# Kernel tuning notes

Measured on AMD Instinct MI355X. Metric: run time of the kernel, lower is better.

The kernel has to match this reference:

```python
import jax, jax.numpy as jnp
import numpy as np

B, N, DIM = 4, 2048, 512
H, DH = 8, 64  # n_heads, dim_head; inner = H*DH = 512
SCALE = DH ** -0.5


def setup_inputs() -> dict:
    key = jax.random.key(0)
    k1, k2, k3 = jax.random.split(key, 3)
    inner = H * DH
    X = jax.random.normal(k1, (B, N, DIM), dtype=jnp.float32)
    W_qkv = jax.random.normal(k2, (DIM, 3 * inner), dtype=jnp.float32) * (DIM ** -0.5)
    W_out = jax.random.normal(k3, (inner, DIM), dtype=jnp.float32) * (inner ** -0.5)
    b_out = jnp.zeros((DIM,), dtype=jnp.float32)
    return {"X": X, "W_qkv": W_qkv, "W_out": W_out, "b_out": b_out}


def reference(X, W_qkv, W_out, b_out):
    # X: (b, n, dim)
    qkv = X @ W_qkv                      # (b, n, 3*h*d)
    q, k, v = jnp.split(qkv, 3, axis=-1)
    def to_heads(t):
        b, n, _ = t.shape
        return t.reshape(b, n, H, DH).transpose(0, 2, 1, 3)  # (b, h, n, d)
    q, k, v = to_heads(q), to_heads(k), to_heads(v)
    # NOTE: original computes scores[n, m] = k_n . q_m and softmaxes over m (query axis)
    scores = jnp.einsum('bhnd,bhmd->bhnm', k, q) * SCALE     # (b, h, n_k, m_q)
    att = jax.nn.softmax(scores, axis=-1)
    # out token axis is the KEY index n: out[n, d] = sum_e att[n, e] * v[e, d]
    out = jnp.einsum('bhne,bhed->bhnd', att, v)              # (b, h, n, d)
    out = out.transpose(0, 2, 1, 3).reshape(X.shape[0], X.shape[1], H * DH)  # (b, n, h*d)
    return out @ W_out + b_out
```

## Files before the change

kernel.cpp:

```cpp
#include <hip/hip_runtime.h>
#include <hip/hip_bf16.h>

typedef __bf16 bf16_t;
typedef bf16_t bf16x8 __attribute__((ext_vector_type(8)));
typedef bf16_t bf16x4v __attribute__((ext_vector_type(4)));
typedef float f32x4 __attribute__((ext_vector_type(4)));
typedef float f32x16 __attribute__((ext_vector_type(16)));
typedef int i32x4 __attribute__((ext_vector_type(4)));

#define B_SZ 4
#define N_TOK 2048
#define DIM 512
#define H_N 8
#define DH 64
#define INNER 512
#define M_ROWS 8192
#define NQKV 1536
#define K_FOLD 0.18033688011112042f

#define GLD_LDS16(gp, lp)                                          \
  __builtin_amdgcn_global_load_lds(                                \
      (const __attribute__((address_space(1))) void*)(gp),         \
      (__attribute__((address_space(3))) void*)(lp), 16, 0, 0)

__device__ __forceinline__ float fexp2(float x) {
#if __has_builtin(__builtin_amdgcn_exp2f)
  return __builtin_amdgcn_exp2f(x);
#else
  float r;
  asm volatile("v_exp_f32 %0, %1\n\ts_nop 1" : "=v"(r) : "v"(x));
  return r;
#endif
}

__device__ __forceinline__ int cvtpk_bf16(float lo, float hi) {
  int r;
  asm("v_cvt_pk_bf16_f32 %0, %1, %2" : "=v"(r) : "v"(lo), "v"(hi));
  return r;
}

__device__ __forceinline__ void permswap32(int& a, int& b) {
  asm volatile("v_permlane32_swap_b32 %0, %1" : "+v"(a), "+v"(b));
}

#define XJOB 1048576
#define WQJOB 786432
#define WOJOB 262144
__global__ void prep_kernel(const float* __restrict__ X, bf16_t* __restrict__ Xb,
                            const float* __restrict__ Wqkv, bf16_t* __restrict__ WqkvT,
                            const float* __restrict__ Wout, bf16_t* __restrict__ WoutT) {
  int i = blockIdx.x * blockDim.x + threadIdx.x;
  if (i < XJOB) {
    float4 f = reinterpret_cast<const float4*>(X)[i];
    bf16x4v o;
    o.x = (bf16_t)f.x; o.y = (bf16_t)f.y; o.z = (bf16_t)f.z; o.w = (bf16_t)f.w;
    reinterpret_cast<bf16x4v*>(Xb)[i] = o;
  } else if (i < XJOB + WQJOB) {
    int t = i - XJOB;
    int r = t / NQKV, c = t - r * NQKV;
    WqkvT[(size_t)c * DIM + r] = (bf16_t)Wqkv[t];
  } else if (i < XJOB + WQJOB + WOJOB) {
    int t = i - (XJOB + WQJOB);
    int r = t >> 9, c = t & 511;
    WoutT[(size_t)c * INNER + r] = (bf16_t)Wout[t];
  }
}

__global__ __launch_bounds__(256) void gemm_qkv_kernel(
    const bf16_t* __restrict__ A, const bf16_t* __restrict__ Bt, int K,
    bf16_t* __restrict__ qb, bf16_t* __restrict__ kb, bf16_t* __restrict__ vtb) {
  __shared__ bf16_t As[128 * 64];
  __shared__ bf16_t Bs[128 * 64];

  const int tid = threadIdx.x;
  const int lane = tid & 63;
  const int wave = tid >> 6;
  const int g = lane >> 4, c = lane & 15;
  const int wm = (wave >> 1) * 64, wn = (wave & 1) * 64;
  const int m0 = blockIdx.x * 128, n0 = blockIdx.y * 128;

  f32x4 acc[4][4] = {};

  for (int k0 = 0; k0 < K; k0 += 64) {
    __syncthreads();
    #pragma unroll
    for (int i = 0; i < 4; ++i) {
      int blk = i * 256 + tid;
      int row = blk >> 3;
      int cb = (blk & 7) ^ (row & 7);
      int base = (i * 256 + wave * 64) * 8;
      GLD_LDS16(A + (size_t)(m0 + row) * K + k0 + cb * 8, &As[base]);
      GLD_LDS16(Bt + (size_t)(n0 + row) * K + k0 + cb * 8, &Bs[base]);
    }
    __syncthreads();
    __builtin_amdgcn_s_setprio(1);
    #pragma unroll
    for (int ks = 0; ks < 2; ++ks) {
      bf16x8 af[4], bfr[4];
      #pragma unroll
      for (int i = 0; i < 4; ++i) {
        af[i] = *reinterpret_cast<const bf16x8*>(
            &As[(wm + i * 16 + c) * 64 + (((ks * 4 + g) ^ (c & 7)) * 8)]);
        bfr[i] = *reinterpret_cast<const bf16x8*>(
            &Bs[(wn + i * 16 + c) * 64 + (((ks * 4 + g) ^ (c & 7)) * 8)]);
      }
      #pragma unroll
      for (int mi = 0; mi < 4; ++mi)
        #pragma unroll
        for (int ni = 0; ni < 4; ++ni)
          acc[mi][ni] = __builtin_amdgcn_mfma_f32_16x16x32_bf16(
              af[mi], bfr[ni], acc[mi][ni], 0, 0, 0);
    }
    __builtin_amdgcn_s_setprio(0);
  }

  #pragma unroll
  for (int mi = 0; mi < 4; ++mi) {
    #pragma unroll
    for (int ni = 0; ni < 4; ++ni) {
      int colg = n0 + wn + ni * 16 + c;
      int s = colg >> 9;
      int hh = (colg >> 6) & 7, dd = colg & 63;
      int rowg0 = m0 + wm + mi * 16 + g * 4;
      int bb = rowg0 >> 11, nn = rowg0 & 2047;
      if (s == 2) {
        bf16x4v pk;
        pk.x = (bf16_t)acc[mi][ni][0];
        pk.y = (bf16_t)acc[mi][ni][1];
        pk.z = (bf16_t)acc[mi][ni][2];
        pk.w = (bf16_t)acc[mi][ni][3];
        *reinterpret_cast<bf16x4v*>(
            &vtb[(((size_t)(bb * H_N + hh)) * DH + dd) * N_TOK + nn]) = pk;
      } else {
        float sc = (s == 1) ? K_FOLD : 1.0f;
        bf16_t* dst = (s == 0) ? qb : kb;
        #pragma unroll
        for (int r = 0; r < 4; ++r)
          dst[(((size_t)(bb * H_N + hh)) * N_TOK + nn + r) * DH + dd] =
              (bf16_t)(acc[mi][ni][r] * sc);
      }
    }
  }
}

__global__ __launch_bounds__(256) void gemm_out_kernel(
    const bf16_t* __restrict__ A, const bf16_t* __restrict__ Bt,
    float* __restrict__ outF, const float* __restrict__ bias) {
  __shared__ bf16_t As[64 * 64];
  __shared__ bf16_t Bs[128 * 64];

  const int tid = threadIdx.x;
  const int lane = tid & 63;
  const int wave = tid >> 6;
  const int g = lane >> 4, c = lane & 15;
  const int wm = (wave >> 1) * 32, wn = (wave & 1) * 64;
  const int m0 = blockIdx.x * 64, n0 = blockIdx.y * 128;

  f32x4 acc[2][4] = {};

  for (int k0 = 0; k0 < DIM; k0 += 64) {
    __syncthreads();
    #pragma unroll
    for (int i = 0; i < 2; ++i) {
      int blk = i * 256 + tid;
      int row = blk >> 3;
      int cb = (blk & 7) ^ (row & 7);
      int base = (i * 256 + wave * 64) * 8;
      GLD_LDS16(A + (size_t)(m0 + row) * DIM + k0 + cb * 8, &As[base]);
    }
    #pragma unroll
    for (int i = 0; i < 4; ++i) {
      int blk = i * 256 + tid;
      int row = blk >> 3;
      int cb = (blk & 7) ^ (row & 7);
      int base = (i * 256 + wave * 64) * 8;
      GLD_LDS16(Bt + (size_t)(n0 + row) * DIM + k0 + cb * 8, &Bs[base]);
    }
    __syncthreads();
    __builtin_amdgcn_s_setprio(1);
    #pragma unroll
    for (int ks = 0; ks < 2; ++ks) {
      bf16x8 af[2], bfr[4];
      #pragma unroll
      for (int i = 0; i < 2; ++i)
        af[i] = *reinterpret_cast<const bf16x8*>(
            &As[(wm + i * 16 + c) * 64 + (((ks * 4 + g) ^ (c & 7)) * 8)]);
      #pragma unroll
      for (int i = 0; i < 4; ++i)
        bfr[i] = *reinterpret_cast<const bf16x8*>(
            &Bs[(wn + i * 16 + c) * 64 + (((ks * 4 + g) ^ (c & 7)) * 8)]);
      #pragma unroll
      for (int mi = 0; mi < 2; ++mi)
        #pragma unroll
        for (int ni = 0; ni < 4; ++ni)
          acc[mi][ni] = __builtin_amdgcn_mfma_f32_16x16x32_bf16(
              af[mi], bfr[ni], acc[mi][ni], 0, 0, 0);
    }
    __builtin_amdgcn_s_setprio(0);
  }

  #pragma unroll
  for (int mi = 0; mi < 2; ++mi) {
    #pragma unroll
    for (int ni = 0; ni < 4; ++ni) {
      int colg = n0 + wn + ni * 16 + c;
      #pragma unroll
      for (int r = 0; r < 4; ++r) {
        int rowg = m0 + wm + mi * 16 + g * 4 + r;
        outF[(size_t)rowg * DIM + colg] = acc[mi][ni][r] + bias[colg];
      }
    }
  }
}

__global__ __launch_bounds__(512, 4) void attn_kernel(
    const bf16_t* __restrict__ Qproj, const bf16_t* __restrict__ Kproj,
    const bf16_t* __restrict__ Vt, bf16_t* __restrict__ att_out) {
  const int glin = blockIdx.x;
  const int xcd = glin & 7;
  const int jj = glin >> 3;
  const int hb = xcd * 4 + (jj >> 4);
  const int rb = jj & 15;
  const int h = hb & 7, b = hb >> 3;

  const size_t hbo = (size_t)(b * H_N + h);
  const bf16_t* Aq = Kproj + hbo * N_TOK * DH;
  const bf16_t* Ak = Qproj + hbo * N_TOK * DH;
  const bf16_t* Av = Vt + hbo * (size_t)(DH * N_TOK);

  const int tid = threadIdx.x, lane = tid & 63, wave = tid >> 6;
  const int nl = lane & 31;
  const int hf = lane >> 5;
  const int grp = wave >> 2;
  const int gw = wave & 3;
  const int r0 = rb * 128, wr0 = gw * 32;
  const int kv0 = grp * 1024;

  __shared__ __align__(16) char smem[65536];
  bf16_t* sKg = (bf16_t*)(smem + grp * 32768);
  bf16_t* sVg = (bf16_t*)(smem + grp * 32768 + 16384);

  bf16x8 qreg[4];
  #pragma unroll
  for (int ks = 0; ks < 4; ++ks)
    qreg[ks] = *reinterpret_cast<const bf16x8*>(
        &Aq[(size_t)(r0 + wr0 + nl) * DH + ks * 16 + hf * 8]);

  f32x16 accO0 = {}, accO1 = {};
  float Lp[4] = {};

  const int gtid = tid & 255;
  auto stage = [&](int buf, int j0) {
    #pragma unroll
    for (int i = 0; i < 2; ++i) {
      int idx = i * 256 + gtid;
      int row = idx >> 3;
      int cb = (idx & 7) ^ (row & 7);
      int base = buf * 4096 + (i * 256 + gw * 64) * 8;
      GLD_LDS16(Ak + (size_t)(j0 + row) * DH + cb * 8, sKg + base);
      GLD_LDS16(Av + (size_t)row * N_TOK + j0 + cb * 8, sVg + base);
    }
  };

  stage(0, kv0);
  __syncthreads();

  constexpr int NT = 16;
  for (int t = 0; t < NT; ++t) {
    if (t + 1 < NT) stage((t + 1) & 1, kv0 + (t + 1) * 64);
    const bf16_t* bK = sKg + (t & 1) * 4096;
    const bf16_t* bV = sVg + (t & 1) * 4096;

    f32x16 aT[2] = {};
    __builtin_amdgcn_s_setprio(1);
    #pragma unroll
    for (int ks = 0; ks < 4; ++ks) {
      #pragma unroll
      for (int mi = 0; mi < 2; ++mi) {
        int rowt = mi * 32 + nl;
        bf16x8 ak = *reinterpret_cast<const bf16x8*>(
            &bK[rowt * 64 + (((ks * 2 + hf) ^ (rowt & 7)) * 8)]);
        aT[mi] = __builtin_amdgcn_mfma_f32_32x32x16_bf16(
            ak, qreg[ks], aT[mi], 0, 0, 0);
      }
    }
    __builtin_amdgcn_s_setprio(0);

    #pragma unroll
    for (int r = 0; r < 16; ++r) {
      float p0 = fexp2(aT[0][r]); aT[0][r] = p0;
      float p1 = fexp2(aT[1][r]); aT[1][r] = p1;
      Lp[r & 3] += p0 + p1;
    }

    i32x4 pk[4];
    #pragma unroll
    for (int ks = 0; ks < 4; ++ks) {
      const int mi = ks >> 1, base = (ks & 1) * 8;
      int a0 = cvtpk_bf16(aT[mi][base + 0], aT[mi][base + 1]);
      int b0 = cvtpk_bf16(aT[mi][base + 4], aT[mi][base + 5]);
      int a1 = cvtpk_bf16(aT[mi][base + 2], aT[mi][base + 3]);
      int b1 = cvtpk_bf16(aT[mi][base + 6], aT[mi][base + 7]);
      permswap32(a0, b0);
      permswap32(a1, b1);
      pk[ks].x = a0; pk[ks].y = a1; pk[ks].z = b0; pk[ks].w = b1;
    }

    __builtin_amdgcn_s_setprio(1);
    #pragma unroll
    for (int ks = 0; ks < 4; ++ks) {
      bf16x8 pfrag = __builtin_bit_cast(bf16x8, pk[ks]);
      int rv0 = nl, rv1 = 32 + nl;
      bf16x8 av0 = *reinterpret_cast<const bf16x8*>(
          &bV[rv0 * 64 + (((ks * 2 + hf) ^ (rv0 & 7)) * 8)]);
      bf16x8 av1 = *reinterpret_cast<const bf16x8*>(
          &bV[rv1 * 64 + (((ks * 2 + hf) ^ (rv1 & 7)) * 8)]);
      accO0 = __builtin_amdgcn_mfma_f32_32x32x16_bf16(av0, pfrag, accO0, 0, 0, 0);
      accO1 = __builtin_amdgcn_mfma_f32_32x32x16_bf16(av1, pfrag, accO1, 0, 0, 0);
    }
    __builtin_amdgcn_s_setprio(0);

    __syncthreads();
  }

  float Lsum = (Lp[0] + Lp[1]) + (Lp[2] + Lp[3]);
  float* mb = (float*)smem;
  const int moff = (gw * 64 + lane) * 36;
  if (grp == 1) {
    #pragma unroll
    for (int r = 0; r < 16; ++r) {
      mb[moff + r] = accO0[r];
      mb[moff + 16 + r] = accO1[r];
    }
    mb[moff + 32] = Lsum;
  }
  __syncthreads();
  if (grp == 0) {
    #pragma unroll
    for (int r = 0; r < 16; ++r) {
      accO0[r] += mb[moff + r];
      accO1[r] += mb[moff + 16 + r];
    }
    float l = Lsum + mb[moff + 32];
    l += __shfl_xor(l, 32);
    float invL = 1.0f / l;
    const int nrow = r0 + wr0 + nl;
    #pragma unroll
    for (int q = 0; q < 4; ++q) {
      int d0a = 8 * q + 4 * hf;
      bf16x4v o;
      o.x = (bf16_t)(accO0[4 * q + 0] * invL);
      o.y = (bf16_t)(accO0[4 * q + 1] * invL);
      o.z = (bf16_t)(accO0[4 * q + 2] * invL);
      o.w = (bf16_t)(accO0[4 * q + 3] * invL);
      *reinterpret_cast<bf16x4v*>(
          &att_out[((size_t)(b * N_TOK) + nrow) * INNER + h * DH + d0a]) = o;
      bf16x4v o2;
      o2.x = (bf16_t)(accO1[4 * q + 0] * invL);
      o2.y = (bf16_t)(accO1[4 * q + 1] * invL);
      o2.z = (bf16_t)(accO1[4 * q + 2] * invL);
      o2.w = (bf16_t)(accO1[4 * q + 3] * invL);
      *reinterpret_cast<bf16x4v*>(
          &att_out[((size_t)(b * N_TOK) + nrow) * INNER + h * DH + 32 + d0a]) = o2;
    }
  }
}


extern "C" void kernel_launch(void* const* d_in, const int* in_sizes, int n_in,
                              void* d_out, int out_size, void* d_ws, size_t ws_size,
                              hipStream_t stream) {
  const float* X    = (const float*)d_in[0];
  const float* Wqkv = (const float*)d_in[1];
  const float* Wout = (const float*)d_in[2];
  const float* bout = (const float*)d_in[3];
  float* out = (float*)d_out;

  char* ws = (char*)d_ws;
  bf16_t* Xb    = (bf16_t*)(ws);
  bf16_t* WqkvT = (bf16_t*)(ws + 8388608);
  bf16_t* WoutT = (bf16_t*)(ws + 9961472);
  bf16_t* Qb    = (bf16_t*)(ws + 10485760);
  bf16_t* Kb    = (bf16_t*)(ws + 18874368);
  bf16_t* Vtb   = (bf16_t*)(ws + 27262976);
  bf16_t* AttO  = (bf16_t*)(ws + 35651584);

  prep_kernel<<<(XJOB + WQJOB + WOJOB + 255) / 256, 256, 0, stream>>>(
      X, Xb, Wqkv, WqkvT, Wout, WoutT);

  dim3 g1(M_ROWS / 128, NQKV / 128);
  gemm_qkv_kernel<<<g1, 256, 0, stream>>>(Xb, WqkvT, DIM, Qb, Kb, Vtb);

  attn_kernel<<<dim3(512), 512, 0, stream>>>(Qb, Kb, Vtb, AttO);

  dim3 g3(M_ROWS / 64, DIM / 128);
  gemm_out_kernel<<<g3, 256, 0, stream>>>(AttO, WoutT, out, bout);
}
```

Before: 83.91 us.

## Swizzle GEMM block order per XCD and compute softmax row sums via MFMA

Both GEMMs switch to a 1D grid whose block index is remapped so that consecutive blocks on the same XCD share A row tiles. This is meant to improve L2 reuse across the chiplet-partitioned caches. The attention kernel drops the per-element VALU accumulation of the softmax denominator and instead adds an extra MFMA against a vector of ones, which also removes a cross-lane shuffle. The extra MFMA adds matrix-core work per tile, and the row sum now accumulates bf16-rounded probabilities, which shifts numerics slightly.

```diff
diff --git a/kernel.cpp b/kernel.cpp
--- a/kernel.cpp
+++ b/kernel.cpp
@@ -77,7 +77,10 @@
   const int wave = tid >> 6;
   const int g = lane >> 4, c = lane & 15;
   const int wm = (wave >> 1) * 64, wn = (wave & 1) * 64;
-  const int m0 = blockIdx.x * 128, n0 = blockIdx.y * 128;
+  const int bid = blockIdx.x;
+  const int xcd = bid & 7, j = bid >> 3;
+  const int m0 = (xcd * 8 + j / 12) * 128;
+  const int n0 = (j % 12) * 128;
 
   f32x4 acc[4][4] = {};
 
@@ -154,7 +157,10 @@
   const int wave = tid >> 6;
   const int g = lane >> 4, c = lane & 15;
   const int wm = (wave >> 1) * 32, wn = (wave & 1) * 64;
-  const int m0 = blockIdx.x * 64, n0 = blockIdx.y * 128;
+  const int bid = blockIdx.x;
+  const int xcd = bid & 7, j = bid >> 3;
+  const int m0 = (xcd * 16 + (j >> 2)) * 64;
+  const int n0 = (j & 3) * 128;
 
   f32x4 acc[2][4] = {};
 
@@ -246,8 +252,12 @@
     qreg[ks] = *reinterpret_cast<const bf16x8*>(
         &Aq[(size_t)(r0 + wr0 + nl) * DH + ks * 16 + hf * 8]);
 
+  bf16x8 ones;
+  #pragma unroll
+  for (int i = 0; i < 8; ++i) ones[i] = (bf16_t)1.0f;
+
   f32x16 accO0 = {}, accO1 = {};
-  float Lp[4] = {};
+  f32x16 accL = {};
 
   const int gtid = tid & 255;
   auto stage = [&](int buf, int j0) {
@@ -288,9 +298,8 @@
 
     #pragma unroll
     for (int r = 0; r < 16; ++r) {
-      float p0 = fexp2(aT[0][r]); aT[0][r] = p0;
-      float p1 = fexp2(aT[1][r]); aT[1][r] = p1;
-      Lp[r & 3] += p0 + p1;
+      aT[0][r] = fexp2(aT[0][r]);
+      aT[1][r] = fexp2(aT[1][r]);
     }
 
     i32x4 pk[4];
@@ -317,15 +326,16 @@
           &bV[rv1 * 64 + (((ks * 2 + hf) ^ (rv1 & 7)) * 8)]);
       accO0 = __builtin_amdgcn_mfma_f32_32x32x16_bf16(av0, pfrag, accO0, 0, 0, 0);
       accO1 = __builtin_amdgcn_mfma_f32_32x32x16_bf16(av1, pfrag, accO1, 0, 0, 0);
+      accL  = __builtin_amdgcn_mfma_f32_32x32x16_bf16(ones, pfrag, accL, 0, 0, 0);
     }
     __builtin_amdgcn_s_setprio(0);
 
     __syncthreads();
   }
 
-  float Lsum = (Lp[0] + Lp[1]) + (Lp[2] + Lp[3]);
+  float Lsum = accL[0];
   float* mb = (float*)smem;
-  const int moff = (gw * 64 + lane) * 36;
+  const int moff = (gw * 64 + lane) * 37;
   if (grp == 1) {
     #pragma unroll
     for (int r = 0; r < 16; ++r) {
@@ -341,9 +351,7 @@
       accO0[r] += mb[moff + r];
       accO1[r] += mb[moff + 16 + r];
     }
-    float l = Lsum + mb[moff + 32];
-    l += __shfl_xor(l, 32);
-    float invL = 1.0f / l;
+    float invL = 1.0f / (Lsum + mb[moff + 32]);
     const int nrow = r0 + wr0 + nl;
     #pragma unroll
     for (int q = 0; q < 4; ++q) {
@@ -388,11 +396,9 @@
   prep_kernel<<<(XJOB + WQJOB + WOJOB + 255) / 256, 256, 0, stream>>>(
       X, Xb, Wqkv, WqkvT, Wout, WoutT);
 
-  dim3 g1(M_ROWS / 128, NQKV / 128);
-  gemm_qkv_kernel<<<g1, 256, 0, stream>>>(Xb, WqkvT, DIM, Qb, Kb, Vtb);
+  gemm_qkv_kernel<<<dim3(768), 256, 0, stream>>>(Xb, WqkvT, DIM, Qb, Kb, Vtb);
 
   attn_kernel<<<dim3(512), 512, 0, stream>>>(Qb, Kb, Vtb, AttO);
 
-  dim3 g3(M_ROWS / 64, DIM / 128);
-  gemm_out_kernel<<<g3, 256, 0, stream>>>(AttO, WoutT, out, bout);
-}
+  gemm_out_kernel<<<dim3(512), 256, 0, stream>>>(AttO, WoutT, out, bout);
+}
```

Result: slower. 86.92 us (+3.6%).
